# Optimization experiments

Hardware: AMD Instinct MI355X
Metric: run time of the kernel (lower is better)

The kernel has to match this reference:

```python
import jax, jax.numpy as jnp
import numpy as np

NUM_HEADS = 16
HEAD_DIM = 128
D_MODEL = 2048
SEQ = 2048
BATCH = 1


def setup_inputs() -> dict:
    key = jax.random.key(0)
    ks = jax.random.split(key, 7)
    s = 0.02
    return {
        "x": jax.random.normal(ks[0], (BATCH, SEQ, D_MODEL), dtype=jnp.float32),
        "q_w": jax.random.normal(ks[1], (D_MODEL, D_MODEL), dtype=jnp.float32) * s,
        "k_w": jax.random.normal(ks[2], (D_MODEL, D_MODEL), dtype=jnp.float32) * s,
        "v_w": jax.random.normal(ks[3], (D_MODEL, D_MODEL), dtype=jnp.float32) * s,
        "o_w": jax.random.normal(ks[4], (D_MODEL, D_MODEL), dtype=jnp.float32) * s,
        "gate_w": jax.random.normal(ks[5], (HEAD_DIM, HEAD_DIM), dtype=jnp.float32) * s,
        "gate_b": jax.random.normal(ks[6], (HEAD_DIM,), dtype=jnp.float32) * s,
    }


def reference(x, q_w, k_w, v_w, o_w, gate_w, gate_b):
    B, S, D = x.shape
    H, Hd = NUM_HEADS, HEAD_DIM
    # QKV projections (nn.Linear: y = x @ W^T), split into heads -> [B,H,S,Hd]
    def proj(w):
        return jnp.einsum('bsd,ed->bse', x, w).reshape(B, S, H, Hd).transpose(0, 2, 1, 3)
    q = proj(q_w)
    k = proj(k_w)
    v = proj(v_w)
    scale = 1.0 / jnp.sqrt(jnp.asarray(Hd, dtype=x.dtype))
    scores = jnp.einsum('bhqd,bhkd->bhqk', q, k) * scale  # [B,H,S,S]
    # causal mask
    causal = jnp.tril(jnp.ones((S, S), dtype=bool))
    scores = jnp.where(causal, scores, jnp.asarray(-1e30, dtype=scores.dtype))
    attn = jax.nn.softmax(scores, axis=-1)
    av = jnp.einsum('bhqk,bhkd->bhqd', attn, v)  # [B,H,S,Hd]
    # learned sigmoid gate computed from q, applied elementwise to attention output
    gate = jax.nn.sigmoid(jnp.einsum('bhqd,ed->bhqe', q, gate_w) + gate_b)
    out = av * gate
    out = out.transpose(0, 2, 1, 3).reshape(B, S, D)
    return jnp.einsum('bsd,ed->bse', out, o_w)
```

## Files before the change

kernel.cpp:

```cpp
#include <hip/hip_runtime.h>
#include <stdint.h>
#include <math.h>

#define DM 2048
#define NH 16
#define HD 128
#define LDQ (3 * DM)

typedef __bf16 bf16;
typedef __attribute__((ext_vector_type(8))) __bf16 bf16x8;
typedef __attribute__((ext_vector_type(4))) float f32x4;
typedef __attribute__((ext_vector_type(2))) unsigned int u32x2;

__device__ __forceinline__ void gload_lds16(const void* g, void* l) {
  __builtin_amdgcn_global_load_lds(
      (const __attribute__((address_space(1))) void*)g,
      (__attribute__((address_space(3))) void*)l,
      16, 0, 0);
}

__device__ __forceinline__ unsigned lds_addr(const void* p) {
  return (unsigned)(size_t)(const __attribute__((address_space(3))) void*)p;
}

template <int OFF>
__device__ __forceinline__ u32x2 tr_read(unsigned va) {
  u32x2 r;
  asm volatile("ds_read_b64_tr_b16 %0, %1 offset:%2"
               : "=v"(r) : "v"(va), "i"(OFF));
  return r;
}

#define TR4(dst, vd)                                        \
  dst[0] = tr_read<0>(vd);   dst[1] = tr_read<512>(vd);     \
  dst[2] = tr_read<1024>(vd); dst[3] = tr_read<1536>(vd);

__global__ __launch_bounds__(256) void cvt6(const float* xs, const float* qws,
                                            const float* kws, const float* vws,
                                            const float* ows, const float* gws,
                                            ushort* xd, ushort* w3d, ushort* owd,
                                            ushort* gwd) {
  const int y = blockIdx.y;
  const float4* s; ushort4* d; int n = (DM * DM) / 4;
  switch (y) {
    case 0: s = (const float4*)xs;  d = (ushort4*)xd;  break;
    case 1: s = (const float4*)qws; d = (ushort4*)w3d; break;
    case 2: s = (const float4*)kws; d = (ushort4*)(w3d + (size_t)DM * DM); break;
    case 3: s = (const float4*)vws; d = (ushort4*)(w3d + (size_t)2 * DM * DM); break;
    case 4: s = (const float4*)ows; d = (ushort4*)owd; break;
    default: s = (const float4*)gws; d = (ushort4*)gwd; n = (HD * HD) / 4; break;
  }
  int i = blockIdx.x * 256 + threadIdx.x;
  if (i >= n) return;
  float4 v = s[i];
  union { bf16 b[4]; ushort4 u; } r;
  r.b[0] = (bf16)v.x; r.b[1] = (bf16)v.y; r.b[2] = (bf16)v.z; r.b[3] = (bf16)v.w;
  d[i] = r.u;
}

__global__ __launch_bounds__(512, 1) void gemm_qkv(const bf16* __restrict__ A,
                                                   const bf16* __restrict__ Bw,
                                                   bf16* __restrict__ C) {
  __shared__ __align__(16) bf16 LA[2][256 * 64];
  __shared__ __align__(16) bf16 LB[2][192 * 64];
  const int tid = threadIdx.x;
  const int w = tid >> 6, l = tid & 63;
  const int wm = w >> 2, wn = w & 3;
  const int fr = l & 15, fg = l >> 4;
  const int bid = blockIdx.x;
  const int xcd = bid & 7, idx = bid >> 3;
  const int bm0 = (idx >> 2) * 256;
  const int bn0 = ((xcd << 2) | (idx & 3)) * 192;

  const int srow = l >> 3;
  const int sunit = (l & 7) ^ srow;
  const bf16* pa = A + (size_t)(bm0 + w * 32 + srow) * DM + sunit * 8;
  const bf16* pb = Bw + (size_t)(bn0 + w * 24 + srow) * DM + sunit * 8;

#define STG(buf, kt)                                                        \
  {                                                                         \
    _Pragma("unroll")                                                       \
    for (int i = 0; i < 4; i++)                                             \
      gload_lds16(pa + (size_t)i * 8 * DM + (kt) * 64,                      \
                  &LA[buf][(w * 32 + i * 8) * 64]);                         \
    _Pragma("unroll")                                                       \
    for (int i = 0; i < 3; i++)                                             \
      gload_lds16(pb + (size_t)i * 8 * DM + (kt) * 64,                      \
                  &LB[buf][(w * 24 + i * 8) * 64]);                         \
  }

  f32x4 acc[8][3] = {};

  STG(0, 0);
  STG(1, 1);
  asm volatile("s_waitcnt vmcnt(7)" ::: "memory");
  __builtin_amdgcn_s_barrier();

  const int sw0 = ((fg) ^ (fr & 7)) << 4;
  const int sw1 = ((4 + fg) ^ (fr & 7)) << 4;

  for (int t = 0; t < 32; ++t) {
    const int cur = t & 1;
    const char* Ab = (const char*)&LA[cur][0];
    const char* Bb = (const char*)&LB[cur][0];

    bf16x8 aA[4], aB[4], bA[3], bB[3];
#pragma unroll
    for (int n = 0; n < 3; n++)
      bA[n] = *(const bf16x8*)(Bb + (wn * 48 + n * 16 + fr) * 128 + sw0);
#pragma unroll
    for (int m = 0; m < 4; m++)
      aA[m] = *(const bf16x8*)(Ab + (wm * 128 + m * 16 + fr) * 128 + sw0);
#pragma unroll
    for (int m = 0; m < 4; m++)
      aB[m] = *(const bf16x8*)(Ab + (wm * 128 + (m + 4) * 16 + fr) * 128 + sw0);
    __builtin_amdgcn_sched_barrier(0);
    __builtin_amdgcn_s_setprio(1);
#pragma unroll
    for (int m = 0; m < 4; m++)
#pragma unroll
      for (int n = 0; n < 3; n++)
        acc[m][n] = __builtin_amdgcn_mfma_f32_16x16x32_bf16(aA[m], bA[n], acc[m][n], 0, 0, 0);
    __builtin_amdgcn_s_setprio(0);
    __builtin_amdgcn_sched_barrier(0);
#pragma unroll
    for (int n = 0; n < 3; n++)
      bB[n] = *(const bf16x8*)(Bb + (wn * 48 + n * 16 + fr) * 128 + sw1);
#pragma unroll
    for (int m = 0; m < 4; m++)
      aA[m] = *(const bf16x8*)(Ab + (wm * 128 + m * 16 + fr) * 128 + sw1);
    __builtin_amdgcn_sched_barrier(0);
    __builtin_amdgcn_s_setprio(1);
#pragma unroll
    for (int m = 0; m < 4; m++)
#pragma unroll
      for (int n = 0; n < 3; n++)
        acc[m + 4][n] = __builtin_amdgcn_mfma_f32_16x16x32_bf16(aB[m], bA[n], acc[m + 4][n], 0, 0, 0);
    __builtin_amdgcn_s_setprio(0);
    __builtin_amdgcn_sched_barrier(0);
#pragma unroll
    for (int m = 0; m < 4; m++)
      aB[m] = *(const bf16x8*)(Ab + (wm * 128 + (m + 4) * 16 + fr) * 128 + sw1);
    __builtin_amdgcn_sched_barrier(0);
    __builtin_amdgcn_s_setprio(1);
#pragma unroll
    for (int m = 0; m < 4; m++)
#pragma unroll
      for (int n = 0; n < 3; n++)
        acc[m][n] = __builtin_amdgcn_mfma_f32_16x16x32_bf16(aA[m], bB[n], acc[m][n], 0, 0, 0);
    __builtin_amdgcn_s_setprio(0);
    __builtin_amdgcn_sched_barrier(0);
    __builtin_amdgcn_s_setprio(1);
#pragma unroll
    for (int m = 0; m < 4; m++)
#pragma unroll
      for (int n = 0; n < 3; n++)
        acc[m + 4][n] = __builtin_amdgcn_mfma_f32_16x16x32_bf16(aB[m], bB[n], acc[m + 4][n], 0, 0, 0);
    __builtin_amdgcn_s_setprio(0);
    __builtin_amdgcn_sched_barrier(0);

    __builtin_amdgcn_s_barrier();
    if (t < 30) {
      STG(cur, t + 2);
      asm volatile("s_waitcnt vmcnt(7)" ::: "memory");
    } else {
      asm volatile("s_waitcnt vmcnt(0)" ::: "memory");
    }
    __builtin_amdgcn_s_barrier();
  }

#pragma unroll
  for (int m = 0; m < 8; m++) {
    const int row0 = bm0 + wm * 128 + m * 16 + fg * 4;
#pragma unroll
    for (int n = 0; n < 3; n++) {
      const int col = bn0 + wn * 48 + n * 16 + fr;
#pragma unroll
      for (int j = 0; j < 4; j++) C[(size_t)(row0 + j) * LDQ + col] = (bf16)acc[m][n][j];
    }
  }
#undef STG
}

template <typename OutT>
__global__ __launch_bounds__(256) void gemm128(const bf16* __restrict__ A,
                                               const bf16* __restrict__ Bw,
                                               OutT* __restrict__ C, int ldc) {
  __shared__ __align__(16) bf16 As[128 * 32];
  __shared__ __align__(16) bf16 Bs[128 * 32];
  const int tid = threadIdx.x;
  const int w = tid >> 6, l = tid & 63;
  const int wr = w >> 1, wc = w & 1;
  const int bx = blockIdx.x, by = blockIdx.y;
  const int lrow = l >> 2, lcol = (l & 3) * 8;
  const int fr = l & 15, fg = l >> 4;
  const bf16* Ag = A + (size_t)(by * 128 + w * 32 + lrow) * DM + lcol;
  const bf16* Bg = Bw + (size_t)(bx * 128 + w * 32 + lrow) * DM + lcol;
  bf16* Asw = &As[(w * 32) * 32];
  bf16* Bsw = &Bs[(w * 32) * 32];
  f32x4 acc[4][4] = {};
  for (int kt = 0; kt < DM / 32; ++kt) {
    const int ko = kt * 32;
    gload_lds16(Ag + ko, Asw);
    gload_lds16(Ag + ko + 16 * DM, Asw + 16 * 32);
    gload_lds16(Bg + ko, Bsw);
    gload_lds16(Bg + ko + 16 * DM, Bsw + 16 * 32);
    __syncthreads();
    bf16x8 af[4], bfr[4];
#pragma unroll
    for (int m = 0; m < 4; m++)
      af[m] = *(const bf16x8*)&As[(wr * 64 + m * 16 + fr) * 32 + fg * 8];
#pragma unroll
    for (int n = 0; n < 4; n++)
      bfr[n] = *(const bf16x8*)&Bs[(wc * 64 + n * 16 + fr) * 32 + fg * 8];
#pragma unroll
    for (int m = 0; m < 4; m++)
#pragma unroll
      for (int n = 0; n < 4; n++)
        acc[m][n] = __builtin_amdgcn_mfma_f32_16x16x32_bf16(af[m], bfr[n], acc[m][n], 0, 0, 0);
    __syncthreads();
  }
#pragma unroll
  for (int m = 0; m < 4; m++) {
    const int row0 = by * 128 + wr * 64 + m * 16 + fg * 4;
#pragma unroll
    for (int n = 0; n < 4; n++) {
      const int col = bx * 128 + wc * 64 + n * 16 + fr;
#pragma unroll
      for (int j = 0; j < 4; j++) C[(size_t)(row0 + j) * ldc + col] = (OutT)acc[m][n][j];
    }
  }
}

__global__ __launch_bounds__(256, 2) void attn_k(const bf16* __restrict__ QKV,
                                                 const bf16* __restrict__ GWb,
                                                 const float* __restrict__ gbias,
                                                 bf16* __restrict__ Gout) {
  __shared__ __align__(16) bf16 Ks[2][8192];
  __shared__ __align__(16) bf16 Vs[2][8192];
  const int gid = blockIdx.x;
  const int h = gid & 15;
  const int idx = gid >> 4;
  const int qt = (idx < 16) ? (31 - idx) : (idx - 16);
  const int tid = threadIdx.x;
  const int w = tid >> 6, l = tid & 63;
  const int fr = l & 15, fg = l >> 4;
  const int fg4 = fg * 4;
  const int qbase = qt * 64 + w * 16;
  const int qg = qbase + fr;
  const int qcol = h * HD;
  const int kcol = DM + h * HD;
  const int vcol = 2 * DM + h * HD;
  const float scale = 0.08838834764831845f;

  bf16x8 bq[4];
#pragma unroll
  for (int kt = 0; kt < 4; kt++)
    bq[kt] = *(const bf16x8*)&QKV[(size_t)(qbase + fr) * LDQ + qcol + kt * 32 + fg * 8];

  const bf16* vbase = QKV + (size_t)(l >> 1) * LDQ + vcol + (l & 1) * 8;
  bf16* Ksl = &Ks[0][0];
  bf16* Vsl = &Vs[0][0];
  const unsigned ldsb = lds_addr(Vsl) + 8u * (unsigned)l;

#define STAGE(buf, kvbase)                                                    \
  {                                                                           \
    _Pragma("unroll")                                                         \
    for (int c = 0; c < 4; c++) {                                             \
      const int i = w * 4 + c;                                                \
      const int krow = i * 4 + (l >> 4);                                      \
      const int c16 = (l & 15) ^ (krow & 7);                                  \
      gload_lds16(QKV + (size_t)((kvbase) + krow) * LDQ + kcol + c16 * 8,     \
                  Ksl + (buf) * 8192 + i * 512);                              \
      const int db = i >> 1, k0 = (i & 1) * 32;                               \
      gload_lds16(vbase + (size_t)((kvbase) + k0) * LDQ + db * 16,            \
                  Vsl + (buf) * 8192 + db * 1024 + k0 * 16);                  \
    }                                                                         \
  }

  f32x4 oacc[8] = {};
  float m = -1e30f, lsum = 0.f;

  STAGE(0, 0);
  __syncthreads();

  for (int t = 0; t <= qt; ++t) {
    const int kv0 = t * 64;
    const int cur = t & 1;
    bf16x8 ak[4][4];
    {
      const char* Kb = (const char*)(Ksl + cur * 8192);
      const int swz = fr & 7;
#pragma unroll
      for (int kb = 0; kb < 4; kb++) {
        const char* rp = Kb + (kb * 16 + fr) * 256;
#pragma unroll
        for (int kt = 0; kt < 4; kt++)
          ak[kb][kt] = *(const bf16x8*)(rp + (((kt * 4 + fg) ^ swz) << 4));
      }
    }
    if (t < qt) STAGE(cur ^ 1, kv0 + 64);
    f32x4 sacc[4] = {};
#pragma unroll
    for (int kb = 0; kb < 4; kb++)
#pragma unroll
      for (int kt = 0; kt < 4; kt++)
        sacc[kb] = __builtin_amdgcn_mfma_f32_16x16x32_bf16(ak[kb][kt], bq[kt], sacc[kb], 0, 0, 0);
    const bool diag = (t == qt);
    float p[4][4];
    float tmax = -1e30f;
#pragma unroll
    for (int kb = 0; kb < 4; kb++)
#pragma unroll
      for (int j = 0; j < 4; j++) {
        float s = sacc[kb][j] * scale;
        if (diag && (kv0 + kb * 16 + fg4 + j) > qg) s = -1e30f;
        p[kb][j] = s;
        tmax = fmaxf(tmax, s);
      }
    tmax = fmaxf(tmax, __shfl_xor(tmax, 16, 64));
    tmax = fmaxf(tmax, __shfl_xor(tmax, 32, 64));
    const float mnew = fmaxf(m, tmax);
    const float alpha = __expf(m - mnew);
    m = mnew;
    float sum = 0.f;
#pragma unroll
    for (int kb = 0; kb < 4; kb++)
#pragma unroll
      for (int j = 0; j < 4; j++) {
        const float e = __expf(p[kb][j] - m);
        p[kb][j] = e;
        sum += e;
      }
    sum += __shfl_xor(sum, 16, 64);
    sum += __shfl_xor(sum, 32, 64);
    lsum = lsum * alpha + sum;
    float alpha4[4];
#pragma unroll
    for (int j = 0; j < 4; j++) alpha4[j] = __shfl(alpha, fg4 + j, 64);
#pragma unroll
    for (int db = 0; db < 8; db++)
#pragma unroll
      for (int j = 0; j < 4; j++) oacc[db][j] *= alpha4[j];
    bf16x8 pa[2];
#pragma unroll
    for (int kc = 0; kc < 2; kc++)
#pragma unroll
      for (int e = 0; e < 8; e++) pa[kc][e] = (bf16)p[2 * kc + (e >> 2)][e & 3];
    {
      const unsigned va = ldsb + (unsigned)cur * 16384u;
      u32x2 ta[4], tb[4];
      TR4(ta, va);
#pragma unroll
      for (int db = 0; db < 8; db++) {
        const u32x2* curp = (db & 1) ? tb : ta;
        u32x2* nxtp = (db & 1) ? ta : tb;
        if (db < 7) {
          const unsigned vd = va + (unsigned)(db + 1) * 2048u;
          TR4(nxtp, vd);
          asm volatile("s_waitcnt lgkmcnt(4)" ::: "memory");
        } else {
          asm volatile("s_waitcnt lgkmcnt(0)" ::: "memory");
        }
        __builtin_amdgcn_sched_barrier(0);
        union { u32x2 h[2]; bf16x8 v; } u0, u1;
        u0.h[0] = curp[0]; u0.h[1] = curp[1];
        u1.h[0] = curp[2]; u1.h[1] = curp[3];
        oacc[db] = __builtin_amdgcn_mfma_f32_16x16x32_bf16(pa[0], u0.v, oacc[db], 0, 0, 0);
        oacc[db] = __builtin_amdgcn_mfma_f32_16x16x32_bf16(pa[1], u1.v, oacc[db], 0, 0, 0);
      }
    }
    __syncthreads();
  }

  const float rinv = 1.0f / lsum;
  float rinv4[4];
#pragma unroll
  for (int j = 0; j < 4; j++) rinv4[j] = __shfl(rinv, fg4 + j, 64);
  f32x4 gacc[8] = {};
#pragma unroll
  for (int kt = 0; kt < 4; kt++)
#pragma unroll
    for (int eb = 0; eb < 8; eb++) {
      const bf16x8 bg = *(const bf16x8*)&GWb[(eb * 16 + fr) * HD + kt * 32 + fg * 8];
      gacc[eb] = __builtin_amdgcn_mfma_f32_16x16x32_bf16(bq[kt], bg, gacc[eb], 0, 0, 0);
    }
#pragma unroll
  for (int db = 0; db < 8; db++) {
    const int e = db * 16 + fr;
    const float bias = gbias[e];
    const int col = h * HD + e;
#pragma unroll
    for (int j = 0; j < 4; j++) {
      const float gate = 1.0f / (1.0f + __expf(-(gacc[db][j] + bias)));
      const float o = oacc[db][j] * rinv4[j] * gate;
      Gout[(size_t)(qbase + fg4 + j) * DM + col] = (bf16)o;
    }
  }
#undef STAGE
}

extern "C" void kernel_launch(void* const* d_in, const int* in_sizes, int n_in,
                              void* d_out, int out_size, void* d_ws, size_t ws_size,
                              hipStream_t stream) {
  const float* x  = (const float*)d_in[0];
  const float* qw = (const float*)d_in[1];
  const float* kw = (const float*)d_in[2];
  const float* vw = (const float*)d_in[3];
  const float* ow = (const float*)d_in[4];
  const float* gw = (const float*)d_in[5];
  const float* gb = (const float*)d_in[6];
  float* out = (float*)d_out;

  char* ws = (char*)d_ws;
  const size_t MB = 1024 * 1024;
  bf16* xb  = (bf16*)(ws + 0 * MB);
  bf16* w3b = (bf16*)(ws + 8 * MB);
  bf16* owb = (bf16*)(ws + 32 * MB);
  bf16* gwb = (bf16*)(ws + 40 * MB);
  bf16* QKV = (bf16*)(ws + 41 * MB);
  bf16* Gb  = (bf16*)(ws + 65 * MB);

  cvt6<<<dim3(4096, 6), 256, 0, stream>>>(x, qw, kw, vw, ow, gw,
                                          (ushort*)xb, (ushort*)w3b,
                                          (ushort*)owb, (ushort*)gwb);

  gemm_qkv<<<256, 512, 0, stream>>>(xb, w3b, QKV);

  attn_k<<<512, 256, 0, stream>>>(QKV, gwb, gb, Gb);

  gemm128<float><<<dim3(16, 16), 256, 0, stream>>>(Gb, owb, out, DM);
}
```

Before: 173.2 us.

## Software-pipeline LDS fragment loads across k-steps in QKV GEMM

Restructures the QKV GEMM main loop so the first-half-k fragments for the next tile are read from LDS right after the barrier, and the second-half fragments are issued before the MFMAs that do not need them, with explicit lgkmcnt waits. This hides LDS read latency behind MFMA work. It also raises the launch-bounds minimum blocks hint to 2, which tightens the register budget. With 8x3 accumulators plus extra fragment registers, that could cause spills, and LDS usage likely prevents two blocks per CU anyway.

```diff
diff --git a/kernel.cpp b/kernel.cpp
--- a/kernel.cpp
+++ b/kernel.cpp
@@ -58,7 +58,7 @@
   d[i] = r.u;
 }
 
-__global__ __launch_bounds__(512, 1) void gemm_qkv(const bf16* __restrict__ A,
+__global__ __launch_bounds__(512, 2) void gemm_qkv(const bf16* __restrict__ A,
                                                    const bf16* __restrict__ Bw,
                                                    bf16* __restrict__ C) {
   __shared__ __align__(16) bf16 LA[2][256 * 64];
@@ -98,64 +98,69 @@
 
   const int sw0 = ((fg) ^ (fr & 7)) << 4;
   const int sw1 = ((4 + fg) ^ (fr & 7)) << 4;
+  const char* AB = (const char*)&LA[0][0];
+  const char* BB = (const char*)&LB[0][0];
+  const int aoff = (wm * 128 + fr) * 128;
+  const int boff = (wn * 48 + fr) * 128;
+
+  bf16x8 bA[3], bB[3], aP[4], aQ[4], aR[4], aS[4];
+
+#pragma unroll
+  for (int n = 0; n < 3; n++) bA[n] = *(const bf16x8*)(BB + boff + n * 2048 + sw0);
+#pragma unroll
+  for (int m = 0; m < 4; m++) aP[m] = *(const bf16x8*)(AB + aoff + m * 2048 + sw0);
+#pragma unroll
+  for (int m = 0; m < 4; m++) aQ[m] = *(const bf16x8*)(AB + aoff + (m + 4) * 2048 + sw0);
+  __builtin_amdgcn_sched_barrier(0);
 
   for (int t = 0; t < 32; ++t) {
     const int cur = t & 1;
-    const char* Ab = (const char*)&LA[cur][0];
-    const char* Bb = (const char*)&LB[cur][0];
-
-    bf16x8 aA[4], aB[4], bA[3], bB[3];
-#pragma unroll
-    for (int n = 0; n < 3; n++)
-      bA[n] = *(const bf16x8*)(Bb + (wn * 48 + n * 16 + fr) * 128 + sw0);
-#pragma unroll
-    for (int m = 0; m < 4; m++)
-      aA[m] = *(const bf16x8*)(Ab + (wm * 128 + m * 16 + fr) * 128 + sw0);
-#pragma unroll
-    for (int m = 0; m < 4; m++)
-      aB[m] = *(const bf16x8*)(Ab + (wm * 128 + (m + 4) * 16 + fr) * 128 + sw0);
+    const char* Ac = AB + cur * 32768;
+    const char* Bc = BB + cur * 24576;
+#pragma unroll
+    for (int n = 0; n < 3; n++) bB[n] = *(const bf16x8*)(Bc + boff + n * 2048 + sw1);
+#pragma unroll
+    for (int m = 0; m < 4; m++) aR[m] = *(const bf16x8*)(Ac + aoff + m * 2048 + sw1);
+    asm volatile("s_waitcnt lgkmcnt(11)" ::: "memory");
     __builtin_amdgcn_sched_barrier(0);
     __builtin_amdgcn_s_setprio(1);
 #pragma unroll
     for (int m = 0; m < 4; m++)
 #pragma unroll
       for (int n = 0; n < 3; n++)
-        acc[m][n] = __builtin_amdgcn_mfma_f32_16x16x32_bf16(aA[m], bA[n], acc[m][n], 0, 0, 0);
+        acc[m][n] = __builtin_amdgcn_mfma_f32_16x16x32_bf16(aP[m], bA[n], acc[m][n], 0, 0, 0);
     __builtin_amdgcn_s_setprio(0);
     __builtin_amdgcn_sched_barrier(0);
 #pragma unroll
-    for (int n = 0; n < 3; n++)
-      bB[n] = *(const bf16x8*)(Bb + (wn * 48 + n * 16 + fr) * 128 + sw1);
-#pragma unroll
-    for (int m = 0; m < 4; m++)
-      aA[m] = *(const bf16x8*)(Ab + (wm * 128 + m * 16 + fr) * 128 + sw1);
+    for (int m = 0; m < 4; m++) aS[m] = *(const bf16x8*)(Ac + aoff + (m + 4) * 2048 + sw1);
+    asm volatile("s_waitcnt lgkmcnt(11)" ::: "memory");
     __builtin_amdgcn_sched_barrier(0);
     __builtin_amdgcn_s_setprio(1);
 #pragma unroll
     for (int m = 0; m < 4; m++)
 #pragma unroll
       for (int n = 0; n < 3; n++)
-        acc[m + 4][n] = __builtin_amdgcn_mfma_f32_16x16x32_bf16(aB[m], bA[n], acc[m + 4][n], 0, 0, 0);
+        acc[m + 4][n] = __builtin_amdgcn_mfma_f32_16x16x32_bf16(aQ[m], bA[n], acc[m + 4][n], 0, 0, 0);
     __builtin_amdgcn_s_setprio(0);
     __builtin_amdgcn_sched_barrier(0);
-#pragma unroll
-    for (int m = 0; m < 4; m++)
-      aB[m] = *(const bf16x8*)(Ab + (wm * 128 + (m + 4) * 16 + fr) * 128 + sw1);
+    asm volatile("s_waitcnt lgkmcnt(4)" ::: "memory");
     __builtin_amdgcn_sched_barrier(0);
     __builtin_amdgcn_s_setprio(1);
 #pragma unroll
     for (int m = 0; m < 4; m++)
 #pragma unroll
       for (int n = 0; n < 3; n++)
-        acc[m][n] = __builtin_amdgcn_mfma_f32_16x16x32_bf16(aA[m], bB[n], acc[m][n], 0, 0, 0);
+        acc[m][n] = __builtin_amdgcn_mfma_f32_16x16x32_bf16(aR[m], bB[n], acc[m][n], 0, 0, 0);
     __builtin_amdgcn_s_setprio(0);
     __builtin_amdgcn_sched_barrier(0);
+    asm volatile("s_waitcnt lgkmcnt(0)" ::: "memory");
+    __builtin_amdgcn_sched_barrier(0);
     __builtin_amdgcn_s_setprio(1);
 #pragma unroll
     for (int m = 0; m < 4; m++)
 #pragma unroll
       for (int n = 0; n < 3; n++)
-        acc[m + 4][n] = __builtin_amdgcn_mfma_f32_16x16x32_bf16(aB[m], bB[n], acc[m + 4][n], 0, 0, 0);
+        acc[m + 4][n] = __builtin_amdgcn_mfma_f32_16x16x32_bf16(aS[m], bB[n], acc[m + 4][n], 0, 0, 0);
     __builtin_amdgcn_s_setprio(0);
     __builtin_amdgcn_sched_barrier(0);
 
@@ -167,6 +172,17 @@
       asm volatile("s_waitcnt vmcnt(0)" ::: "memory");
     }
     __builtin_amdgcn_s_barrier();
+    if (t < 31) {
+      const char* An = AB + (cur ^ 1) * 32768;
+      const char* Bn = BB + (cur ^ 1) * 24576;
+#pragma unroll
+      for (int n = 0; n < 3; n++) bA[n] = *(const bf16x8*)(Bn + boff + n * 2048 + sw0);
+#pragma unroll
+      for (int m = 0; m < 4; m++) aP[m] = *(const bf16x8*)(An + aoff + m * 2048 + sw0);
+#pragma unroll
+      for (int m = 0; m < 4; m++) aQ[m] = *(const bf16x8*)(An + aoff + (m + 4) * 2048 + sw0);
+    }
+    __builtin_amdgcn_sched_barrier(0);
   }
 
 #pragma unroll
```

New measurement: 171.6 us. No clear change (-0.9%).
